# Performance work log

Hardware: AMD Instinct MI355X
Metric: run time of the kernel (lower is better)

## Reference

```python
import jax, jax.numpy as jnp
import numpy as np

N_FLOWS = 20
DIM = 4
BATCH = 8388608  # 2**23 samples -> 128 MB fp32 input


def setup_inputs() -> dict:
    key = jax.random.key(0)
    k1, k2, k3, k4 = jax.random.split(key, 4)
    return {
        "X": jax.random.normal(k1, (BATCH, DIM), dtype=jnp.float32),
        "x0s": jax.random.normal(k2, (N_FLOWS, DIM), dtype=jnp.float32),
        "alpha_primes": jax.random.normal(k3, (N_FLOWS,), dtype=jnp.float32),
        "beta_primes": jax.random.normal(k4, (N_FLOWS,), dtype=jnp.float32),
    }


def reference(X, x0s, alpha_primes, beta_primes):
    """Chain of 20 pyro-style Radial flow transforms on dim-4 vectors.

    Each flow: alpha = softplus(alpha'), beta = -alpha + softplus(beta')
               y = x + beta * (x - x0) / (alpha + ||x - x0||)
    """
    def step(x, params):
        x0, a_p, b_p = params
        alpha = jax.nn.softplus(a_p)                 # scalar > 0
        beta = -alpha + jax.nn.softplus(b_p)         # beta >= -alpha (invertibility)
        diff = x - x0                                # [B, 4]
        r = jnp.linalg.norm(diff, axis=-1, keepdims=True)  # [B, 1]
        return x + beta * diff / (alpha + r), None

    X, _ = jax.lax.scan(step, X, (x0s, alpha_primes, beta_primes))
    return X
```

## Files before the change

kernel.cpp:

```cpp
#include <hip/hip_runtime.h>

#define N_FLOWS 20
#define DIM 4
#define ITEMS 4
#define BLOCK 256
#define PBLOCKS 2048
#define TILE (BLOCK * ITEMS)

typedef float v2f __attribute__((ext_vector_type(2)));
typedef float v4f __attribute__((ext_vector_type(4)));

#define SB __builtin_amdgcn_sched_barrier(0)

__global__ void radial_setup(const float* __restrict__ x0s,
                             const float* __restrict__ alpha_primes,
                             const float* __restrict__ beta_primes,
                             float* __restrict__ ws) {
    int f = threadIdx.x;
    if (f < N_FLOWS) {
        float alpha = __logf(1.0f + __expf(alpha_primes[f]));
        float beta  = __logf(1.0f + __expf(beta_primes[f])) - alpha;
        float* p = ws + 8 * f;
        const bool last = (f == N_FLOWS - 1);
#pragma unroll
        for (int j = 0; j < 4; ++j)
            p[j] = x0s[4 * f + j] - (last ? 0.0f : x0s[4 * (f + 1) + j]);
        p[4] = alpha;
        p[5] = beta;
        p[6] = 0.0f;
        p[7] = 0.0f;
    } else if (f == N_FLOWS) {
        float* p = ws + 8 * N_FLOWS;
        p[0] = x0s[0]; p[1] = x0s[1]; p[2] = x0s[2]; p[3] = x0s[3];
        p[4] = 0.0f; p[5] = 0.0f; p[6] = 0.0f; p[7] = 0.0f;
    }
}

#define FLOWQ(F)                                                               \
    do {                                                                       \
        float4 c  = P[2 * (F)];                         \
        float4 ab = P[2 * (F) + 1];                                            \
        v2f c01 = (v2f){c.x, c.y};                                             \
        v2f c23 = (v2f){c.z, c.w};                                             \
        float alpha = ab.x, beta = ab.y;                                       \
        v2f q0 = a0 * a0; q0 += b0 * b0;                                       \
        v2f q1 = a1 * a1; q1 += b1 * b1;                                       \
        v2f q2 = a2 * a2; q2 += b2 * b2;                                       \
        v2f q3 = a3 * a3; q3 += b3 * b3;                                       \
        float D0 = alpha + __builtin_amdgcn_sqrtf(q0.x + q0.y);                \
        float D1 = alpha + __builtin_amdgcn_sqrtf(q1.x + q1.y);                \
        float D2 = alpha + __builtin_amdgcn_sqrtf(q2.x + q2.y);                \
        float D3 = alpha + __builtin_amdgcn_sqrtf(q3.x + q3.y);                \
        float p1  = D0 * D1;                                                   \
        float p2  = p1 * D2;                                                   \
        float p3  = p2 * D3;                                                   \
        float inv = __builtin_amdgcn_rcpf(p3);                                 \
        float i3 = inv * p2;                                         \
        float w2 = inv * D3;                                 \
        float i2 = w2 * p1;                                          \
        float w1 = w2 * D2;                                     \
        float i1 = w1 * D0;                                          \
        float i0 = w1 * D1;                                          \
        float s0 = __builtin_fmaf(beta, i0, 1.0f);                             \
        float s1 = __builtin_fmaf(beta, i1, 1.0f);                             \
        float s2 = __builtin_fmaf(beta, i2, 1.0f);                             \
        float s3 = __builtin_fmaf(beta, i3, 1.0f);                             \
        v2f sv;                                                                \
        sv = (v2f){s0, s0}; a0 = sv * a0 + c01; b0 = sv * b0 + c23;            \
        sv = (v2f){s1, s1}; a1 = sv * a1 + c01; b1 = sv * b1 + c23;            \
        sv = (v2f){s2, s2}; a2 = sv * a2 + c01; b2 = sv * b2 + c23;            \
        sv = (v2f){s3, s3}; a3 = sv * a3 + c01; b3 = sv * b3 + c23;            \
    } while (0)

#define DINIT(V0, V1, V2, V3)                                                  \
    do {                                                                       \
        a0 = (v2f){V0.x, V0.y} - z01; b0 = (v2f){V0.z, V0.w} - z23;            \
        a1 = (v2f){V1.x, V1.y} - z01; b1 = (v2f){V1.z, V1.w} - z23;            \
        a2 = (v2f){V2.x, V2.y} - z01; b2 = (v2f){V2.z, V2.w} - z23;            \
        a3 = (v2f){V3.x, V3.y} - z01; b3 = (v2f){V3.z, V3.w} - z23;            \
    } while (0)

#define STORES(IDXV)                                                           \
    do {                                                                       \
        v4f o;                                                                 \
        o = (v4f){a0.x, a0.y, b0.x, b0.y};                                     \
        __builtin_nontemporal_store(o, Ovv + (IDXV));                          \
        o = (v4f){a1.x, a1.y, b1.x, b1.y};                                     \
        __builtin_nontemporal_store(o, Ovv + (IDXV) + BLOCK);                  \
        o = (v4f){a2.x, a2.y, b2.x, b2.y};                                     \
        __builtin_nontemporal_store(o, Ovv + (IDXV) + 2 * BLOCK);              \
        o = (v4f){a3.x, a3.y, b3.x, b3.y};                                     \
        __builtin_nontemporal_store(o, Ovv + (IDXV) + 3 * BLOCK);              \
    } while (0)

#define PHASE(V0, V1, V2, V3, N0, N1, N2, N3)                                  \
    do {                                                                       \
        unsigned nidx = idx + ((t + 1 < T) ? (unsigned)TILE : 0u);             \
        DINIT(V0, V1, V2, V3);                                                 \
        FLOWQ(0);                                                              \
        SB; N0 = Xv[nidx]; SB;                                                 \
        FLOWQ(1); FLOWQ(2); FLOWQ(3); FLOWQ(4); FLOWQ(5);                      \
        SB; N1 = Xv[nidx + BLOCK]; SB;                                         \
        FLOWQ(6); FLOWQ(7); FLOWQ(8); FLOWQ(9); FLOWQ(10);                     \
        SB; N2 = Xv[nidx + 2 * BLOCK]; SB;                                     \
        FLOWQ(11); FLOWQ(12); FLOWQ(13); FLOWQ(14); FLOWQ(15);                 \
        SB; N3 = Xv[nidx + 3 * BLOCK]; SB;                                     \
        FLOWQ(16); FLOWQ(17); FLOWQ(18); FLOWQ(19);                            \
        STORES(idx);                                                           \
    } while (0)

__global__ __launch_bounds__(BLOCK) void radial_main(
    const float4* __restrict__ Xv,
    const float4* __restrict__ P,
    float4* __restrict__ Ov,
    int T)
{
    v4f* __restrict__ Ovv = (v4f*)Ov;

    float4 z = P[2 * N_FLOWS];
    v2f z01 = (v2f){z.x, z.y};
    v2f z23 = (v2f){z.z, z.w};

    const unsigned lane = threadIdx.x;
    unsigned idx = (unsigned)blockIdx.x * (unsigned)T * TILE + lane;

    float4 A0, A1, A2, A3, B0, B1, B2, B3;
    v2f a0, a1, a2, a3, b0, b1, b2, b3;

    A0 = Xv[idx];
    A1 = Xv[idx + BLOCK];
    A2 = Xv[idx + 2 * BLOCK];
    A3 = Xv[idx + 3 * BLOCK];

    int t = 0;
    for (;;) {
        PHASE(A0, A1, A2, A3, B0, B1, B2, B3);
        if (++t >= T) break;
        idx += TILE;
        PHASE(B0, B1, B2, B3, A0, A1, A2, A3);
        if (++t >= T) break;
        idx += TILE;
    }
}

__global__ void radial_tail(const float4* __restrict__ Xv,
                            const float4* __restrict__ P,
                            float4* __restrict__ Ov,
                            int start, int batch) {
    int idx = start + blockIdx.x * blockDim.x + threadIdx.x;
    if (idx >= batch) return;
    float4 z = P[2 * N_FLOWS];
    float4 v = Xv[idx];
    float dx = v.x - z.x, dy = v.y - z.y, dz = v.z - z.z, dw = v.w - z.w;
#pragma unroll
    for (int f = 0; f < N_FLOWS; ++f) {
        float4 c  = P[2 * f];
        float4 ab = P[2 * f + 1];
        float r2 = dx * dx + dy * dy + dz * dz + dw * dw;
        float r  = __builtin_amdgcn_sqrtf(r2);
        float s  = __builtin_fmaf(ab.y, __builtin_amdgcn_rcpf(ab.x + r), 1.0f);
        dx = s * dx + c.x; dy = s * dy + c.y;
        dz = s * dz + c.z; dw = s * dw + c.w;
    }
    float4 o; o.x = dx; o.y = dy; o.z = dz; o.w = dw;
    Ov[idx] = o;
}

extern "C" void kernel_launch(void* const* d_in, const int* in_sizes, int n_in,
                              void* d_out, int out_size, void* d_ws, size_t ws_size,
                              hipStream_t stream) {
    const float* X   = (const float*)d_in[0];
    const float* x0s = (const float*)d_in[1];
    const float* ap  = (const float*)d_in[2];
    const float* bp  = (const float*)d_in[3];
    float* out = (float*)d_out;
    float* ws  = (float*)d_ws;

    int batch = in_sizes[0] / DIM;
    int tiles = batch / TILE;

    radial_setup<<<1, 64, 0, stream>>>(x0s, ap, bp, ws);

    int done = 0;
    if (tiles >= PBLOCKS) {
        int T = tiles / PBLOCKS;
        radial_main<<<PBLOCKS, BLOCK, 0, stream>>>(
            (const float4*)X, (const float4*)ws, (float4*)out, T);
        done = PBLOCKS * T * TILE;
    } else if (tiles > 0) {
        radial_main<<<tiles, BLOCK, 0, stream>>>(
            (const float4*)X, (const float4*)ws, (float4*)out, 1);
        done = tiles * TILE;
    }

    int rem = batch - done;
    if (rem > 0)
        radial_tail<<<(rem + 255) / 256, 256, 0, stream>>>(
            (const float4*)X, (const float4*)ws, (float4*)out, done, batch);
}
```

Before: 248.9 us.

## Stage input tiles through LDS with async global-to-LDS copies

Replaces the register double-buffered prefetch with asynchronous global_load_lds copies into two shared-memory buffers. Each thread then reads its samples back from LDS and runs the 20 flows. Items per thread drop from 4 to 2, so the flow math batches two reciprocals instead of four. The aim is to overlap the next tile's load with compute while freeing registers, at the cost of less ILP per thread, an extra LDS round trip, and reliance on correct implicit waits before the LDS reads.

```diff
diff --git a/kernel.cpp b/kernel.cpp
--- a/kernel.cpp
+++ b/kernel.cpp
@@ -2,7 +2,7 @@
 
 #define N_FLOWS 20
 #define DIM 4
-#define ITEMS 4
+#define ITEMS 2
 #define BLOCK 256
 #define PBLOCKS 2048
 #define TILE (BLOCK * ITEMS)
@@ -10,7 +10,12 @@
 typedef float v2f __attribute__((ext_vector_type(2)));
 typedef float v4f __attribute__((ext_vector_type(4)));
 
-#define SB __builtin_amdgcn_sched_barrier(0)
+__device__ __forceinline__ void async_cp16(const float4* g, float4* l) {
+    __builtin_amdgcn_global_load_lds(
+        (__attribute__((address_space(1))) void*)(float4*)g,
+        (__attribute__((address_space(3))) void*)l,
+        16, 0, 0);
+}
 
 __global__ void radial_setup(const float* __restrict__ x0s,
                              const float* __restrict__ alpha_primes,
@@ -36,77 +41,47 @@
     }
 }
 
-#define FLOWQ(F)                                                               \
+#define FLOWP(F)                                                               \
     do {                                                                       \
         float4 c  = P[2 * (F)];                         \
         float4 ab = P[2 * (F) + 1];                                            \
         v2f c01 = (v2f){c.x, c.y};                                             \
         v2f c23 = (v2f){c.z, c.w};                                             \
-        float alpha = ab.x, beta = ab.y;                                       \
         v2f q0 = a0 * a0; q0 += b0 * b0;                                       \
         v2f q1 = a1 * a1; q1 += b1 * b1;                                       \
-        v2f q2 = a2 * a2; q2 += b2 * b2;                                       \
-        v2f q3 = a3 * a3; q3 += b3 * b3;                                       \
-        float D0 = alpha + __builtin_amdgcn_sqrtf(q0.x + q0.y);                \
-        float D1 = alpha + __builtin_amdgcn_sqrtf(q1.x + q1.y);                \
-        float D2 = alpha + __builtin_amdgcn_sqrtf(q2.x + q2.y);                \
-        float D3 = alpha + __builtin_amdgcn_sqrtf(q3.x + q3.y);                \
-        float p1  = D0 * D1;                                                   \
-        float p2  = p1 * D2;                                                   \
-        float p3  = p2 * D3;                                                   \
-        float inv = __builtin_amdgcn_rcpf(p3);                                 \
-        float i3 = inv * p2;                                         \
-        float w2 = inv * D3;                                 \
-        float i2 = w2 * p1;                                          \
-        float w1 = w2 * D2;                                     \
-        float i1 = w1 * D0;                                          \
-        float i0 = w1 * D1;                                          \
-        float s0 = __builtin_fmaf(beta, i0, 1.0f);                             \
-        float s1 = __builtin_fmaf(beta, i1, 1.0f);                             \
-        float s2 = __builtin_fmaf(beta, i2, 1.0f);                             \
-        float s3 = __builtin_fmaf(beta, i3, 1.0f);                             \
+        float D0 = ab.x + __builtin_amdgcn_sqrtf(q0.x + q0.y);                 \
+        float D1 = ab.x + __builtin_amdgcn_sqrtf(q1.x + q1.y);                 \
+        float inv = __builtin_amdgcn_rcpf(D0 * D1);                            \
+        float s0 = __builtin_fmaf(ab.y, inv * D1, 1.0f);                       \
+        float s1 = __builtin_fmaf(ab.y, inv * D0, 1.0f);                       \
         v2f sv;                                                                \
         sv = (v2f){s0, s0}; a0 = sv * a0 + c01; b0 = sv * b0 + c23;            \
         sv = (v2f){s1, s1}; a1 = sv * a1 + c01; b1 = sv * b1 + c23;            \
-        sv = (v2f){s2, s2}; a2 = sv * a2 + c01; b2 = sv * b2 + c23;            \
-        sv = (v2f){s3, s3}; a3 = sv * a3 + c01; b3 = sv * b3 + c23;            \
     } while (0)
 
-#define DINIT(V0, V1, V2, V3)                                                  \
+#define COMPSTORE(SRCBUF, IDXV)                                                \
     do {                                                                       \
-        a0 = (v2f){V0.x, V0.y} - z01; b0 = (v2f){V0.z, V0.w} - z23;            \
-        a1 = (v2f){V1.x, V1.y} - z01; b1 = (v2f){V1.z, V1.w} - z23;            \
-        a2 = (v2f){V2.x, V2.y} - z01; b2 = (v2f){V2.z, V2.w} - z23;            \
-        a3 = (v2f){V3.x, V3.y} - z01; b3 = (v2f){V3.z, V3.w} - z23;            \
-    } while (0)
-
-#define STORES(IDXV)                                                           \
-    do {                                                                       \
+        float4 v0 = SRCBUF[tid];                                               \
+        float4 v1 = SRCBUF[tid + BLOCK];                                       \
+        v2f a0 = (v2f){v0.x, v0.y} - z01;                                      \
+        v2f b0 = (v2f){v0.z, v0.w} - z23;                                      \
+        v2f a1 = (v2f){v1.x, v1.y} - z01;                                      \
+        v2f b1 = (v2f){v1.z, v1.w} - z23;                                      \
+        FLOWP(0);  FLOWP(1);  FLOWP(2);  FLOWP(3);  FLOWP(4);                  \
+        FLOWP(5);  FLOWP(6);  FLOWP(7);  FLOWP(8);  FLOWP(9);                  \
+        FLOWP(10); FLOWP(11); FLOWP(12); FLOWP(13); FLOWP(14);                 \
+        FLOWP(15); FLOWP(16); FLOWP(17); FLOWP(18); FLOWP(19);                 \
         v4f o;                                                                 \
         o = (v4f){a0.x, a0.y, b0.x, b0.y};                                     \
         __builtin_nontemporal_store(o, Ovv + (IDXV));                          \
         o = (v4f){a1.x, a1.y, b1.x, b1.y};                                     \
         __builtin_nontemporal_store(o, Ovv + (IDXV) + BLOCK);                  \
-        o = (v4f){a2.x, a2.y, b2.x, b2.y};                                     \
-        __builtin_nontemporal_store(o, Ovv + (IDXV) + 2 * BLOCK);              \
-        o = (v4f){a3.x, a3.y, b3.x, b3.y};                                     \
-        __builtin_nontemporal_store(o, Ovv + (IDXV) + 3 * BLOCK);              \
     } while (0)
 
-#define PHASE(V0, V1, V2, V3, N0, N1, N2, N3)                                  \
+#define STAGE(DSTBUF, NIDX)                                                    \
     do {                                                                       \
-        unsigned nidx = idx + ((t + 1 < T) ? (unsigned)TILE : 0u);             \
-        DINIT(V0, V1, V2, V3);                                                 \
-        FLOWQ(0);                                                              \
-        SB; N0 = Xv[nidx]; SB;                                                 \
-        FLOWQ(1); FLOWQ(2); FLOWQ(3); FLOWQ(4); FLOWQ(5);                      \
-        SB; N1 = Xv[nidx + BLOCK]; SB;                                         \
-        FLOWQ(6); FLOWQ(7); FLOWQ(8); FLOWQ(9); FLOWQ(10);                     \
-        SB; N2 = Xv[nidx + 2 * BLOCK]; SB;                                     \
-        FLOWQ(11); FLOWQ(12); FLOWQ(13); FLOWQ(14); FLOWQ(15);                 \
-        SB; N3 = Xv[nidx + 3 * BLOCK]; SB;                                     \
-        FLOWQ(16); FLOWQ(17); FLOWQ(18); FLOWQ(19);                            \
-        STORES(idx);                                                           \
+        async_cp16(Xv + (NIDX),         &DSTBUF[tid]);                         \
+        async_cp16(Xv + (NIDX) + BLOCK, &DSTBUF[tid + BLOCK]);                 \
     } while (0)
 
 __global__ __launch_bounds__(BLOCK) void radial_main(
@@ -115,29 +90,34 @@
     float4* __restrict__ Ov,
     int T)
 {
+    __shared__ float4 bufA[TILE];
+    __shared__ float4 bufB[TILE];
+
     v4f* __restrict__ Ovv = (v4f*)Ov;
 
     float4 z = P[2 * N_FLOWS];
     v2f z01 = (v2f){z.x, z.y};
     v2f z23 = (v2f){z.z, z.w};
 
-    const unsigned lane = threadIdx.x;
-    unsigned idx = (unsigned)blockIdx.x * (unsigned)T * TILE + lane;
+    const unsigned tid = threadIdx.x;
+    unsigned idx = (unsigned)blockIdx.x * (unsigned)T * TILE + tid;
 
-    float4 A0, A1, A2, A3, B0, B1, B2, B3;
-    v2f a0, a1, a2, a3, b0, b1, b2, b3;
-
-    A0 = Xv[idx];
-    A1 = Xv[idx + BLOCK];
-    A2 = Xv[idx + 2 * BLOCK];
-    A3 = Xv[idx + 3 * BLOCK];
+    STAGE(bufA, idx);
 
     int t = 0;
     for (;;) {
-        PHASE(A0, A1, A2, A3, B0, B1, B2, B3);
+        {
+            unsigned nidx = idx + ((t + 1 < T) ? (unsigned)TILE : 0u);
+            STAGE(bufB, nidx);
+            COMPSTORE(bufA, idx);
+        }
         if (++t >= T) break;
         idx += TILE;
-        PHASE(B0, B1, B2, B3, A0, A1, A2, A3);
+        {
+            unsigned nidx = idx + ((t + 1 < T) ? (unsigned)TILE : 0u);
+            STAGE(bufA, nidx);
+            COMPSTORE(bufB, idx);
+        }
         if (++t >= T) break;
         idx += TILE;
     }
```

New measurement: 251.5 us. About the same (+1.0%).
